# Kernel tuning notes

Measured on AMD Instinct MI355X. Metric: run time of the kernel, lower is better.

Reference implementation:

```python
import jax, jax.numpy as jnp
import numpy as np

IMG_SIZE = 500
FM = 31
RATIOS = [1.0, 2.0, 0.5]
SCALES = [128, 256, 512]
PRE_NMS_TOPN = 1000
POST_NMS_TOPN = 256
IOU_THR = 0.8
VARIANCES = np.array([0.1, 0.1, 0.2, 0.2], np.float32)
BATCH = 64
TOTAL_ANCHORS = FM * FM * len(RATIOS) * len(SCALES)  # 8649


def _generate_anchors():
    # mimics bbox_utils.generate_anchors: normalized grid centers + base sizes
    stride = 1.0 / FM
    ctr = (np.arange(FM, dtype=np.float32) / FM) + stride / 2.0
    gy, gx = np.meshgrid(ctr, ctr, indexing="ij")
    base = []
    for scale in SCALES:
        for ratio in RATIOS:
            w = scale * np.sqrt(ratio) / IMG_SIZE
            h = scale / np.sqrt(ratio) / IMG_SIZE
            base.append([-h / 2, -w / 2, h / 2, w / 2])
    base = np.array(base, np.float32)                        # [9, 4]
    ctrs = np.stack([gy, gx, gy, gx], -1).reshape(-1, 1, 4)  # [FM*FM, 1, 4]
    anc = (ctrs + base[None]).reshape(-1, 4)                 # [8649, 4] yxyx
    return np.clip(anc, 0.0, 1.0)


def setup_inputs() -> dict:
    key = jax.random.key(0)
    k1, k2, k3 = jax.random.split(key, 3)
    return {
        "rpn_bbox_deltas": jax.random.normal(k1, (BATCH, TOTAL_ANCHORS, 4), jnp.float32),
        "rpn_probs": jax.random.uniform(k2, (BATCH, TOTAL_ANCHORS), dtype=jnp.float32),
        "gt_labels": jax.random.randint(k3, (BATCH, 10), 0, 21, jnp.int32),
        "anchors": jnp.asarray(_generate_anchors()),
    }


def _delta_to_bbox(anchors, deltas):
    # anchors [A,4] yxyx broadcast against deltas [B,A,4] (ty,tx,th,tw)
    ah = anchors[..., 2] - anchors[..., 0]
    aw = anchors[..., 3] - anchors[..., 1]
    acy = anchors[..., 0] + 0.5 * ah
    acx = anchors[..., 1] + 0.5 * aw
    h = jnp.exp(deltas[..., 2]) * ah
    w = jnp.exp(deltas[..., 3]) * aw
    cy = deltas[..., 0] * ah + acy
    cx = deltas[..., 1] * aw + acx
    return jnp.stack([cy - 0.5 * h, cx - 0.5 * w, cy + 0.5 * h, cx + 0.5 * w], axis=-1)


def _pairwise_iou(b):
    # b [N,4] yxyx -> [N,N]
    area = (b[:, 2] - b[:, 0]) * (b[:, 3] - b[:, 1])
    y1 = jnp.maximum(b[:, None, 0], b[None, :, 0])
    x1 = jnp.maximum(b[:, None, 1], b[None, :, 1])
    y2 = jnp.minimum(b[:, None, 2], b[None, :, 2])
    x2 = jnp.minimum(b[:, None, 3], b[None, :, 3])
    inter = jnp.maximum(y2 - y1, 0.0) * jnp.maximum(x2 - x1, 0.0)
    union = area[:, None] + area[None, :] - inter
    return inter / jnp.maximum(union, 1e-8)


def _nms_single(boxes, scores):
    # boxes [N,4] already sorted by descending score (from top_k);
    # greedy NMS matching single-class tf.image.combined_non_max_suppression
    n = boxes.shape[0]
    iou = _pairwise_iou(boxes)
    idx = jnp.arange(n)

    def body(keep, i):
        sup = keep[i] & (iou[i] > IOU_THR) & (idx > i)
        return keep & ~sup, None

    keep, _ = jax.lax.scan(body, jnp.ones((n,), bool), jnp.arange(n))
    masked = jnp.where(keep, scores, -1.0)  # scores are probs >= 0
    sel_scores, sel_idx = jax.lax.top_k(masked, POST_NMS_TOPN)
    sel_boxes = jnp.clip(boxes[sel_idx], 0.0, 1.0)  # combined NMS clips boxes
    valid = sel_scores >= 0.0
    return (jnp.where(valid[:, None], sel_boxes, 0.0),
            jnp.where(valid, sel_scores, 0.0))


def reference(rpn_bbox_deltas, rpn_probs, gt_labels, anchors):
    deltas = rpn_bbox_deltas * jnp.asarray(VARIANCES)          # [B,A,4]
    rpn_bboxes = _delta_to_bbox(anchors[None], deltas)         # [B,A,4]
    pre_scores, pre_idx = jax.lax.top_k(rpn_probs, PRE_NMS_TOPN)  # [B,1000]
    pre_boxes = jnp.take_along_axis(rpn_bboxes, pre_idx[..., None], axis=1)
    roi_bboxes, roi_scores = jax.vmap(_nms_single)(pre_boxes, pre_scores)
    return roi_bboxes, roi_scores  # [B,256,4], [B,256]
```

## Files before the change

### kernel.cpp

```cpp
#include <hip/hip_runtime.h>
#include <math.h>

#define BATCH 64
#define A_TOTAL 8649
#define PRE 1000
#define POST 256
#define NBINS 4096
#define NW 16
#define TRI_WORDS 7680

__global__ __launch_bounds__(1024) void k_topk_decode(
    const float* __restrict__ deltas,
    const float* __restrict__ probs,
    const float* __restrict__ anchors,
    float4* __restrict__ tboxes,
    float* __restrict__ tscores,
    float* __restrict__ tareas)
{
    #pragma clang fp contract(off)
    const int b = blockIdx.x;
    const int t = threadIdx.x;
    __shared__ unsigned int hist[NBINS];
    __shared__ unsigned int exc[NBINS];
    __shared__ unsigned long long cand[2048];
    __shared__ unsigned int gsum[256];
    __shared__ unsigned int s_thr;
    __shared__ unsigned int s_n;

    for (int i = t; i < NBINS; i += 1024) hist[i] = 0u;
    __syncthreads();

    const float* pr = probs + (size_t)b * A_TOTAL;
    for (int i = t; i < A_TOTAL; i += 1024) {
        unsigned int bits = __float_as_uint(pr[i]);
        atomicAdd(&hist[bits >> 18], 1u);
    }
    __syncthreads();

    if (t < 256) {
        unsigned int gs = 0;
        #pragma unroll
        for (int q = 0; q < 16; ++q) gs += hist[t * 16 + q];
        gsum[t] = gs;
    }
    __syncthreads();
    if (t < 64) {
        const int l = t;
        unsigned int a  = gsum[4 * l];
        unsigned int b2 = gsum[4 * l + 1];
        unsigned int c  = gsum[4 * l + 2];
        unsigned int d  = gsum[4 * l + 3];
        unsigned int quad = a + b2 + c + d;
        unsigned int q = quad;
        #pragma unroll
        for (int off = 1; off < 64; off <<= 1) {
            unsigned int v = __shfl_down(q, off);
            q += (l + off < 64) ? v : 0u;
        }
        gsum[4 * l]     = q;
        gsum[4 * l + 1] = q - a;
        gsum[4 * l + 2] = q - a - b2;
        gsum[4 * l + 3] = q - a - b2 - c;
    }
    __syncthreads();
    if (t < 256) {
        unsigned int run = (t == 255) ? 0u : gsum[t + 1];
        for (int q = 15; q >= 0; --q) {
            int bin = t * 16 + q;
            exc[bin] = run;
            run += hist[bin];
        }
    }
    __syncthreads();
    for (int bin = t; bin < NBINS; bin += 1024) {
        unsigned int ge = exc[bin] + hist[bin];
        unsigned int ge1 = (bin == NBINS - 1) ? 0u : (exc[bin + 1] + hist[bin + 1]);
        if (ge >= PRE && ge1 < PRE) { s_thr = (unsigned int)bin; s_n = ge; }
    }
    __syncthreads();
    const unsigned int T = s_thr;
    const int n = (s_n > 2048u) ? 2048 : (int)s_n;
    for (int i = t; i < NBINS; i += 1024) hist[i] = 0u;
    __syncthreads();

    for (int i = t; i < A_TOTAL; i += 1024) {
        unsigned int bits = __float_as_uint(pr[i]);
        unsigned int bin = bits >> 18;
        if (bin >= T) {
            unsigned int p = exc[bin] + atomicAdd(&hist[bin], 1u);
            if (p < 2048u)
                cand[p] = ((unsigned long long)bits << 32) |
                          (unsigned long long)(0xFFFFFFFFu - (unsigned int)i);
        }
    }
    __syncthreads();

    const float4* anc4 = (const float4*)anchors;
    const float4* dl4  = (const float4*)(deltas + (size_t)b * A_TOTAL * 4);
    for (int p = t; p < n; p += 1024) {
        unsigned long long key = cand[p];
        unsigned int bin = (unsigned int)(key >> 50);
        int segs = (int)exc[bin];
        int sege = (bin > 0) ? (int)exc[bin - 1] : n;
        if (sege > 2048) sege = 2048;
        unsigned int rank = (unsigned int)segs;
        for (int q = segs; q < sege; ++q) rank += (cand[q] > key);
        if (rank >= PRE) continue;
        unsigned int idx = 0xFFFFFFFFu - (unsigned int)(key & 0xFFFFFFFFull);
        float sc = __uint_as_float((unsigned int)(key >> 32));
        float4 a = anc4[idx];
        float4 d = dl4[idx];
        float ah  = a.z - a.x;
        float aw  = a.w - a.y;
        float acy = a.x + 0.5f * ah;
        float acx = a.y + 0.5f * aw;
        float ty = d.x * 0.1f, tx = d.y * 0.1f, th = d.z * 0.2f, tw = d.w * 0.2f;
        float h = (float)exp((double)th) * ah;
        float w = (float)exp((double)tw) * aw;
        float cy = ty * ah + acy;
        float cx = tx * aw + acx;
        float4 bx = make_float4(cy - 0.5f * h, cx - 0.5f * w, cy + 0.5f * h, cx + 0.5f * w);
        tboxes[(size_t)b * PRE + rank] = bx;
        tscores[(size_t)b * PRE + rank] = sc;
        tareas[(size_t)b * PRE + rank] = (bx.z - bx.x) * (bx.w - bx.y);
    }
}

__global__ __launch_bounds__(256) void k_masks(
    const float4* __restrict__ tboxes,
    const float* __restrict__ tareas,
    unsigned long long* __restrict__ masks)
{
    #pragma clang fp contract(off)
    const int b = blockIdx.y;
    int f = blockIdx.x * 4 + (threadIdx.x >> 6);
    f = __builtin_amdgcn_readfirstlane(f);
    int I = 0;
    while (f >= 16 - I) { f -= 16 - I; ++I; }
    const int W = I + f;
    const int lane = threadIdx.x & 63;
    const int row = (I << 6) + lane;
    const int rr = (row < PRE) ? row : 0;
    const float4 bi = tboxes[(size_t)b * PRE + rr];
    const float areai = tareas[(size_t)b * PRE + rr];
    const float4* __restrict__ bjp = tboxes + (size_t)b * PRE + (W << 6);
    const float*  __restrict__ ajp = tareas + (size_t)b * PRE + (W << 6);
    const int jmax = (PRE - (W << 6) < 64) ? (PRE - (W << 6)) : 64;
    const double C = (double)0.8f + 0x1p-25;
    const bool diag = (I == W);
    unsigned int mlo = 0u, mhi = 0u;

#define IOU_SUP(jj, sup) do { \
        const float4 bj = bjp[jj]; \
        const float aj = ajp[jj]; \
        float y1 = fmaxf(bi.x, bj.x); \
        float x1 = fmaxf(bi.y, bj.y); \
        float y2 = fminf(bi.z, bj.z); \
        float x2 = fminf(bi.w, bj.w); \
        float inter = fmaxf(y2 - y1, 0.0f) * fmaxf(x2 - x1, 0.0f); \
        float uni = (areai + aj) - inter;             \
        float u = fmaxf(uni, 1e-8f); \
        sup = ((double)inter >= C * (double)u);       \
        if (diag) sup = sup && (lane < (jj)); \
    } while (0)

    if (jmax == 64) {
        #pragma unroll 4
        for (int jj = 0; jj < 32; ++jj) {
            bool sup; IOU_SUP(jj, sup);
            mlo |= sup ? (1u << jj) : 0u;
        }
        #pragma unroll 4
        for (int jj = 32; jj < 64; ++jj) {
            bool sup; IOU_SUP(jj, sup);
            mhi |= sup ? (1u << (jj - 32)) : 0u;
        }
    } else {
        for (int jj = 0; jj < jmax; ++jj) {
            bool sup; IOU_SUP(jj, sup);
            unsigned int s = sup ? (1u << (jj & 31)) : 0u;
            if (jj < 32) mlo |= s; else mhi |= s;
        }
    }
#undef IOU_SUP
    if (row < PRE)
        masks[((size_t)b * PRE + (size_t)row) * NW + W] =
            ((unsigned long long)mhi << 32) | (unsigned long long)mlo;
}

__global__ __launch_bounds__(256) void k_nms_out(
    const float4* __restrict__ tboxes,
    const float* __restrict__ tscores,
    const unsigned long long* __restrict__ masks,
    float* __restrict__ out)
{
    #pragma clang fp contract(off)
    const int b = blockIdx.x;
    const int tid = threadIdx.x;
    const unsigned long long* Mb = masks + (size_t)b * PRE * NW;
    __shared__ unsigned long long Ml[TRI_WORDS];
    __shared__ int sidx[POST];
    __shared__ int s_kc;

    unsigned int dlo[NW], dhi[NW];
    if (tid < 64) {
        const int lane = tid;
        #pragma unroll
        for (int W = 0; W < NW; ++W) {
            const int base = W << 6;
            const int nvalid = (PRE - base < 64) ? (PRE - base) : 64;
            const int drow = base + ((lane < nvalid) ? lane : 0);
            unsigned long long dv = Mb[(size_t)drow * NW + W];
            if (lane >= nvalid) dv = 0ull;
            dlo[W] = (unsigned int)dv;
            dhi[W] = (unsigned int)(dv >> 32);
        }
    }

    #pragma unroll
    for (int I = 0; I < 15; ++I) {
        const int cnt = 15 - I;
        const int base = 64 * (15 * I - (I * (I - 1)) / 2);
        const int total = 64 * cnt;
        for (int idx = tid; idx < total; idx += 256) {
            const int r = (I << 6) + idx / cnt;
            const int w = I + 1 + (idx % cnt);
            Ml[base + idx] = Mb[(size_t)r * NW + w];
        }
    }
    __syncthreads();

    if (tid < 64) {
        const int lane = tid;
        const int wword = lane & 15;
        const int wgrp  = lane >> 4;
        unsigned long long rm = 0ull;
        int kc = 0;
        bool done = false;
        #pragma unroll
        for (int W = 0; W < NW; ++W) {
            const int base = W << 6;
            unsigned int rlo = (unsigned int)__builtin_amdgcn_readlane((int)(unsigned int)rm, W)
                             | (unsigned int)__builtin_amdgcn_readlane((int)(unsigned int)rm, W + 16)
                             | (unsigned int)__builtin_amdgcn_readlane((int)(unsigned int)rm, W + 32)
                             | (unsigned int)__builtin_amdgcn_readlane((int)(unsigned int)rm, W + 48);
            unsigned int rhi = (unsigned int)__builtin_amdgcn_readlane((int)(unsigned int)(rm >> 32), W)
                             | (unsigned int)__builtin_amdgcn_readlane((int)(unsigned int)(rm >> 32), W + 16)
                             | (unsigned int)__builtin_amdgcn_readlane((int)(unsigned int)(rm >> 32), W + 32)
                             | (unsigned int)__builtin_amdgcn_readlane((int)(unsigned int)(rm >> 32), W + 48);
            unsigned long long rmW = ((unsigned long long)rhi << 32) | (unsigned long long)rlo;
            unsigned long long valid = (PRE - base >= 64) ? ~0ull : ((1ull << (PRE - base)) - 1ull);
            unsigned long long alive = ~rmW & valid;
            unsigned long long keptw = 0ull;
            while (alive) {
                int i = __builtin_amdgcn_readfirstlane(__ffsll(alive) - 1);
                keptw |= (1ull << i);
                if (lane == 0) sidx[kc] = base + i;
                ++kc;
                if (kc == POST) { done = true; break; }
                unsigned int dl = (unsigned int)__builtin_amdgcn_readlane((int)dlo[W], i);
                unsigned int dh = (unsigned int)__builtin_amdgcn_readlane((int)dhi[W], i);
                unsigned long long d = ((unsigned long long)dh << 32) | (unsigned long long)dl;
                alive &= ~(d | (1ull << i));
            }
            if (done) break;
            const int cntW = 15 - W;
            const int baseW = 64 * (15 * W - (W * (W - 1)) / 2);
            unsigned long long kw = keptw;
            while (kw) {
                unsigned long long tA = kw;
                if (wgrp > 0) tA &= tA - 1ull;
                if (wgrp > 1) tA &= tA - 1ull;
                if (wgrp > 2) tA &= tA - 1ull;
                const bool vA = (tA != 0ull);
                const int iA = vA ? (__ffsll(tA) - 1) : 0;
                unsigned long long kw2 = kw;
                kw2 &= kw2 - 1ull; kw2 &= kw2 - 1ull; kw2 &= kw2 - 1ull; kw2 &= kw2 - 1ull;
                unsigned long long tB = kw2;
                if (wgrp > 0) tB &= tB - 1ull;
                if (wgrp > 1) tB &= tB - 1ull;
                if (wgrp > 2) tB &= tB - 1ull;
                const bool vB = (tB != 0ull);
                const int iB = vB ? (__ffsll(tB) - 1) : 0;
                kw = kw2;
                kw &= kw - 1ull; kw &= kw - 1ull; kw &= kw - 1ull; kw &= kw - 1ull;
                unsigned long long lA = 0ull, lB = 0ull;
                if (wword > W) {
                    lA = Ml[baseW + iA * cntW + (wword - W - 1)];
                    lB = Ml[baseW + iB * cntW + (wword - W - 1)];
                }
                unsigned long long gA =
                    ((unsigned long long)(unsigned int)__builtin_amdgcn_readlane((int)dhi[W], iA) << 32)
                  |  (unsigned long long)(unsigned int)__builtin_amdgcn_readlane((int)dlo[W], iA);
                unsigned long long gB =
                    ((unsigned long long)(unsigned int)__builtin_amdgcn_readlane((int)dhi[W], iB) << 32)
                  |  (unsigned long long)(unsigned int)__builtin_amdgcn_readlane((int)dlo[W], iB);
                unsigned long long mA = (wword > W) ? lA : ((wword == W) ? gA : 0ull);
                unsigned long long mB = (wword > W) ? lB : ((wword == W) ? gB : 0ull);
                if (!vA) mA = 0ull;
                if (!vB) mB = 0ull;
                rm |= mA | mB;
            }
        }
        if (tid == 0) s_kc = kc;
    }
    __syncthreads();

    const int kc = s_kc;
    const float4* bb = tboxes + (size_t)b * PRE;
    const float* ss = tscores + (size_t)b * PRE;
    float4* oB = (float4*)out + (size_t)b * POST;
    float* oS = out + (size_t)BATCH * POST * 4 + (size_t)b * POST;
    for (int t2 = tid; t2 < POST; t2 += 256) {
        float4 v = make_float4(0.f, 0.f, 0.f, 0.f);
        float sc = 0.f;
        if (t2 < kc) {
            int r = sidx[t2];
            float4 bx = bb[r];
            v.x = fminf(fmaxf(bx.x, 0.f), 1.f);
            v.y = fminf(fmaxf(bx.y, 0.f), 1.f);
            v.z = fminf(fmaxf(bx.z, 0.f), 1.f);
            v.w = fminf(fmaxf(bx.w, 0.f), 1.f);
            sc = ss[r];
        }
        oB[t2] = v;
        oS[t2] = sc;
    }
}

extern "C" void kernel_launch(void* const* d_in, const int* in_sizes, int n_in,
                              void* d_out, int out_size, void* d_ws, size_t ws_size,
                              hipStream_t stream) {
    const float* deltas  = (const float*)d_in[0];
    const float* probs   = (const float*)d_in[1];
    const float* anchors = (const float*)d_in[3];
    float* out = (float*)d_out;

    char* ws = (char*)d_ws;
    float4* tboxes = (float4*)ws;
    float* tscores = (float*)(ws + 1024000);
    unsigned long long* masks = (unsigned long long*)(ws + 1280000);
    float* tareas = (float*)(ws + 9472000);

    k_topk_decode<<<dim3(BATCH), dim3(1024), 0, stream>>>(deltas, probs, anchors,
                                                          tboxes, tscores, tareas);
    k_masks<<<dim3(34, BATCH), dim3(256), 0, stream>>>(tboxes, tareas, masks);
    k_nms_out<<<dim3(BATCH), dim3(256), 0, stream>>>(tboxes, tscores, masks, out);
}
```

Measured before the change: 97.88 us.

## Store NMS masks in packed triangular layout and cache probs in LDS

The suppression masks are now written by k_masks into two buffers. One is a compact diagonal-block array; the other is a column-major packed upper-triangle array padded to 65 entries per column. This lets k_nms_out load the triangle into shared memory with contiguous 16-byte copies using 512 threads, with no strided gather and index divide/modulo, and the padding is meant to reduce LDS bank conflicts on the per-kept-row reads. The top-k kernel also keeps the probability bits in shared memory, so the second pass no longer re-reads global memory. The cost is about 35 KB of extra LDS in the top-k kernel, which may limit occupancy, and a changed workspace layout.

```diff
diff --git a/kernel.cpp b/kernel.cpp
--- a/kernel.cpp
+++ b/kernel.cpp
@@ -7,7 +7,9 @@
 #define POST 256
 #define NBINS 4096
 #define NW 16
-#define TRI_WORDS 7680
+#define TRIG 120
+#define TRIP 65
+#define TRI_WORDS (TRIG * TRIP)
 
 __global__ __launch_bounds__(1024) void k_topk_decode(
     const float* __restrict__ deltas,
@@ -22,6 +24,7 @@
     const int t = threadIdx.x;
     __shared__ unsigned int hist[NBINS];
     __shared__ unsigned int exc[NBINS];
+    __shared__ unsigned int sbits[A_TOTAL];
     __shared__ unsigned long long cand[2048];
     __shared__ unsigned int gsum[256];
     __shared__ unsigned int s_thr;
@@ -33,6 +36,7 @@
     const float* pr = probs + (size_t)b * A_TOTAL;
     for (int i = t; i < A_TOTAL; i += 1024) {
         unsigned int bits = __float_as_uint(pr[i]);
+        sbits[i] = bits;
         atomicAdd(&hist[bits >> 18], 1u);
     }
     __syncthreads();
@@ -84,7 +88,7 @@
     __syncthreads();
 
     for (int i = t; i < A_TOTAL; i += 1024) {
-        unsigned int bits = __float_as_uint(pr[i]);
+        unsigned int bits = sbits[i];
         unsigned int bin = bits >> 18;
         if (bin >= T) {
             unsigned int p = exc[bin] + atomicAdd(&hist[bin], 1u);
@@ -129,7 +133,8 @@
 __global__ __launch_bounds__(256) void k_masks(
     const float4* __restrict__ tboxes,
     const float* __restrict__ tareas,
-    unsigned long long* __restrict__ masks)
+    unsigned long long* __restrict__ mtri,
+    unsigned long long* __restrict__ mdiag)
 {
     #pragma clang fp contract(off)
     const int b = blockIdx.y;
@@ -183,50 +188,51 @@
         }
     }
 #undef IOU_SUP
-    if (row < PRE)
-        masks[((size_t)b * PRE + (size_t)row) * NW + W] =
-            ((unsigned long long)mhi << 32) | (unsigned long long)mlo;
+    const unsigned long long mword =
+        ((unsigned long long)mhi << 32) | (unsigned long long)mlo;
+    if (row < PRE) {
+        if (diag) {
+            mdiag[((size_t)b << 10) + (W << 6) + lane] = mword;
+        } else {
+            const int cg = 15 * I - (I * (I - 1)) / 2 + (W - I - 1);
+            mtri[(size_t)b * TRI_WORDS + (size_t)cg * TRIP + lane] = mword;
+        }
+    }
 }
 
-__global__ __launch_bounds__(256) void k_nms_out(
+__global__ __launch_bounds__(512) void k_nms_out(
     const float4* __restrict__ tboxes,
     const float* __restrict__ tscores,
-    const unsigned long long* __restrict__ masks,
+    const unsigned long long* __restrict__ mtri,
+    const unsigned long long* __restrict__ mdiag,
     float* __restrict__ out)
 {
     #pragma clang fp contract(off)
     const int b = blockIdx.x;
     const int tid = threadIdx.x;
-    const unsigned long long* Mb = masks + (size_t)b * PRE * NW;
-    __shared__ unsigned long long Ml[TRI_WORDS];
+    __shared__ __align__(16) unsigned long long Ml[TRI_WORDS];
     __shared__ int sidx[POST];
     __shared__ int s_kc;
 
     unsigned int dlo[NW], dhi[NW];
     if (tid < 64) {
         const int lane = tid;
+        const unsigned long long* Db = mdiag + ((size_t)b << 10);
         #pragma unroll
         for (int W = 0; W < NW; ++W) {
             const int base = W << 6;
             const int nvalid = (PRE - base < 64) ? (PRE - base) : 64;
-            const int drow = base + ((lane < nvalid) ? lane : 0);
-            unsigned long long dv = Mb[(size_t)drow * NW + W];
+            unsigned long long dv = Db[base + lane];
             if (lane >= nvalid) dv = 0ull;
             dlo[W] = (unsigned int)dv;
             dhi[W] = (unsigned int)(dv >> 32);
         }
     }
 
-    #pragma unroll
-    for (int I = 0; I < 15; ++I) {
-        const int cnt = 15 - I;
-        const int base = 64 * (15 * I - (I * (I - 1)) / 2);
-        const int total = 64 * cnt;
-        for (int idx = tid; idx < total; idx += 256) {
-            const int r = (I << 6) + idx / cnt;
-            const int w = I + 1 + (idx % cnt);
-            Ml[base + idx] = Mb[(size_t)r * NW + w];
-        }
+    {
+        const float4* src = (const float4*)(mtri + (size_t)b * TRI_WORDS);
+        float4* dst = (float4*)Ml;
+        for (int idx = tid; idx < TRI_WORDS / 2; idx += 512) dst[idx] = src[idx];
     }
     __syncthreads();
 
@@ -264,8 +270,7 @@
                 alive &= ~(d | (1ull << i));
             }
             if (done) break;
-            const int cntW = 15 - W;
-            const int baseW = 64 * (15 * W - (W * (W - 1)) / 2);
+            const int cgW = 15 * W - (W * (W - 1)) / 2;
             unsigned long long kw = keptw;
             while (kw) {
                 unsigned long long tA = kw;
@@ -286,8 +291,9 @@
                 kw &= kw - 1ull; kw &= kw - 1ull; kw &= kw - 1ull; kw &= kw - 1ull;
                 unsigned long long lA = 0ull, lB = 0ull;
                 if (wword > W) {
-                    lA = Ml[baseW + iA * cntW + (wword - W - 1)];
-                    lB = Ml[baseW + iB * cntW + (wword - W - 1)];
+                    const int col = cgW + (wword - W - 1);
+                    lA = Ml[col * TRIP + iA];
+                    lB = Ml[col * TRIP + iB];
                 }
                 unsigned long long gA =
                     ((unsigned long long)(unsigned int)__builtin_amdgcn_readlane((int)dhi[W], iA) << 32)
@@ -311,7 +317,7 @@
     const float* ss = tscores + (size_t)b * PRE;
     float4* oB = (float4*)out + (size_t)b * POST;
     float* oS = out + (size_t)BATCH * POST * 4 + (size_t)b * POST;
-    for (int t2 = tid; t2 < POST; t2 += 256) {
+    for (int t2 = tid; t2 < POST; t2 += 512) {
         float4 v = make_float4(0.f, 0.f, 0.f, 0.f);
         float sc = 0.f;
         if (t2 < kc) {
@@ -339,11 +345,12 @@
     char* ws = (char*)d_ws;
     float4* tboxes = (float4*)ws;
     float* tscores = (float*)(ws + 1024000);
-    unsigned long long* masks = (unsigned long long*)(ws + 1280000);
-    float* tareas = (float*)(ws + 9472000);
+    float* tareas  = (float*)(ws + 1280000);
+    unsigned long long* mdiag = (unsigned long long*)(ws + 1536000);
+    unsigned long long* mtri  = (unsigned long long*)(ws + 2060288);
 
     k_topk_decode<<<dim3(BATCH), dim3(1024), 0, stream>>>(deltas, probs, anchors,
                                                           tboxes, tscores, tareas);
-    k_masks<<<dim3(34, BATCH), dim3(256), 0, stream>>>(tboxes, tareas, masks);
-    k_nms_out<<<dim3(BATCH), dim3(256), 0, stream>>>(tboxes, tscores, masks, out);
+    k_masks<<<dim3(34, BATCH), dim3(256), 0, stream>>>(tboxes, tareas, mtri, mdiag);
+    k_nms_out<<<dim3(BATCH), dim3(512), 0, stream>>>(tboxes, tscores, mtri, mdiag, out);
 }
```

Result: faster. 89.30 us (median of 2 runs) (-8.8%).
